# Kernel optimization log

Hardware: AMD Instinct MI355X
Metric: run time of the kernel (lower is better)

Reference implementation:

```python
import jax, jax.numpy as jnp
import numpy as np

B, S, D_IN, D_OUT = 4, 2048, 4096, 4096
R, E, SPLIT = 16, 4, 32
SCALING = 32.0 / 16.0  # lora_alpha / r


def setup_inputs() -> dict:
    key = jax.random.key(0)
    ks = jax.random.split(key, 9)
    x = jax.random.normal(ks[0], (B, S, D_IN), dtype=jnp.float32)
    w_base = jax.random.normal(ks[1], (D_OUT, D_IN), dtype=jnp.float32) * (1.0 / np.sqrt(D_IN))
    b_base = jax.random.normal(ks[2], (D_OUT,), dtype=jnp.float32) * 0.01
    w_router_img = jax.random.normal(ks[3], (E, D_IN), dtype=jnp.float32) * 1e-5
    b_router_img = jnp.zeros((E,), dtype=jnp.float32)
    w_router_text = jax.random.normal(ks[4], (E, D_IN), dtype=jnp.float32) * 1e-5
    b_router_text = jnp.zeros((E,), dtype=jnp.float32)
    # per-expert LoRA factors: A_e: [r, D_in], B_e: [D_out, r]
    lora_A = jax.random.normal(ks[5], (E, R, D_IN), dtype=jnp.float32) * (1.0 / np.sqrt(D_IN))
    lora_B = jax.random.normal(ks[6], (E, D_OUT, R), dtype=jnp.float32) * 0.02
    return {
        "x": x, "w_base": w_base, "b_base": b_base,
        "w_router_img": w_router_img, "b_router_img": b_router_img,
        "w_router_text": w_router_text, "b_router_text": b_router_text,
        "lora_A": lora_A, "lora_B": lora_B,
    }


def reference(x, w_base, b_base, w_router_img, b_router_img,
              w_router_text, b_router_text, lora_A, lora_B):
    # base linear: [B,S,D_out]
    base = jnp.einsum("bsd,od->bso", x, w_base) + b_base

    # modality routing: first SPLIT tokens are image, rest text
    x_img, x_text = x[:, :SPLIT], x[:, SPLIT:]
    logits_img = jnp.einsum("bsd,ed->bse", x_img, w_router_img) + b_router_img
    logits_text = jnp.einsum("bsd,ed->bse", x_text, w_router_text) + b_router_text
    gate = jax.nn.softmax(jnp.concatenate([logits_img, logits_text], axis=1), axis=-1)  # [B,S,E]

    # low-rank expert branches: h[b,s,e,r] = x @ A_e^T
    h = jnp.einsum("bsd,erd->bser", x, lora_A)
    h = h * gate[..., None]  # weight each expert's rank-r activation by its gate
    lora_out = jnp.einsum("bser,eor->bso", h, lora_B) * SCALING

    return base + lora_out
```

## Files before the change

kernel.cpp:

```cpp
#include <hip/hip_runtime.h>
#include <hip/hip_bf16.h>

#define D_IN   4096
#define D_OUT  4096
#define NTOK   8192
#define SEQ    2048
#define ER     64

typedef float        f32x4  __attribute__((ext_vector_type(4)));
typedef unsigned int u32x4  __attribute__((ext_vector_type(4)));
typedef unsigned int u32x2  __attribute__((ext_vector_type(2)));
typedef short        s16x8  __attribute__((ext_vector_type(8)));
typedef __bf16       bf16x8 __attribute__((ext_vector_type(8)));
typedef _Float16     f16x8  __attribute__((ext_vector_type(8)));

__device__ inline unsigned f2bf1(float f){
    unsigned u = __builtin_bit_cast(unsigned, f);
    return (u + 0x7fffu + ((u >> 16) & 1u)) >> 16;
}
__device__ inline unsigned pack2(float a, float b){ return f2bf1(a) | (f2bf1(b) << 16); }
__device__ inline f32x4 mfma_bf16(s16x8 a, s16x8 b, f32x4 c){
    return __builtin_amdgcn_mfma_f32_16x16x32_bf16(
        __builtin_bit_cast(bf16x8, a), __builtin_bit_cast(bf16x8, b), c, 0, 0, 0);
}
__device__ inline f32x4 mfma16(s16x8 a, s16x8 b, f32x4 c){
    return __builtin_amdgcn_mfma_f32_16x16x32_f16(
        __builtin_bit_cast(f16x8, a), __builtin_bit_cast(f16x8, b), c, 0, 0, 0);
}

__global__ __launch_bounds__(256) void convert_w_kernel(
    const float* __restrict__ w, _Float16* __restrict__ wh)
{
    size_t i = ((size_t)blockIdx.x * 256 + threadIdx.x) * 8;
    f32x4 a = *(const f32x4*)(w + i);
    f32x4 c = *(const f32x4*)(w + i + 4);
    f16x8 h;
    #pragma unroll
    for (int j = 0; j < 4; ++j){ h[j] = (_Float16)a[j]; h[4+j] = (_Float16)c[j]; }
    *(f16x8*)(wh + i) = h;
}

__global__ __launch_bounds__(256) void lora_c_kernel(
    const float* __restrict__ x,
    const float* __restrict__ wr_img, const float* __restrict__ br_img,
    const float* __restrict__ wr_txt, const float* __restrict__ br_txt,
    const float* __restrict__ lA,
    _Float16* __restrict__ xh, float* __restrict__ c_ws)
{
    __shared__ short xs[16][136];
    __shared__ short bs[80][136];
    __shared__ float lg[16][4];

    const int tid  = threadIdx.x;
    const int lane = tid & 63;
    const int wid  = tid >> 6;
    const int t0   = blockIdx.x * 16;
    const bool img = ((t0 % SEQ) < 32);
    const float* wrr = img ? wr_img : wr_txt;
    const float* br  = img ? br_img : br_txt;

    for (int idx = tid; idx < 816; idx += 256)
        ((unsigned*)&bs[68][0])[idx] = 0u;

    const int xr  = tid >> 4;
    const int xc8 = (tid & 15) * 8;
    const int lr  = tid >> 2;
    const int lc  = (tid & 3) * 4;
    const int rrow = tid >> 5;
    const int rcol = (tid & 31) * 4;

    f32x4 rx0, rx1, rb[8], rv = {0.f,0.f,0.f,0.f};
    rx0 = *(const f32x4*)(x + (size_t)(t0 + xr) * D_IN + xc8);
    rx1 = *(const f32x4*)(x + (size_t)(t0 + xr) * D_IN + xc8 + 4);
    #pragma unroll
    for (int j = 0; j < 8; ++j) rb[j] = *(const f32x4*)(lA + (size_t)lr * D_IN + lc + j*16);
    if (tid < 128) rv = *(const f32x4*)(wrr + (size_t)rrow * D_IN + rcol);

    f32x4 acc0 = {0,0,0,0}, accR0 = {0,0,0,0};
    const int fr = lane & 15, fq = lane >> 4;

    for (int ks = 0; ks < 32; ++ks){
        __syncthreads();
        *(u32x4*)&xs[xr][xc8] = (u32x4){pack2(rx0[0],rx0[1]), pack2(rx0[2],rx0[3]),
                                        pack2(rx1[0],rx1[1]), pack2(rx1[2],rx1[3])};
        #pragma unroll
        for (int j = 0; j < 8; ++j)
            *(u32x2*)&bs[lr][lc + j*16] = (u32x2){pack2(rb[j][0],rb[j][1]), pack2(rb[j][2],rb[j][3])};
        if (tid < 128)
            *(u32x2*)&bs[64 + rrow][rcol] = (u32x2){pack2(rv[0],rv[1]), pack2(rv[2],rv[3])};
        __syncthreads();
        {
            f16x8 h;
            #pragma unroll
            for (int j = 0; j < 4; ++j){ h[j] = (_Float16)rx0[j]; h[4+j] = (_Float16)rx1[j]; }
            *(f16x8*)(xh + (size_t)(t0 + xr) * D_IN + ks*128 + xc8) = h;
        }
        if (ks < 31){
            const int ko = (ks + 1) * 128;
            rx0 = *(const f32x4*)(x + (size_t)(t0 + xr) * D_IN + ko + xc8);
            rx1 = *(const f32x4*)(x + (size_t)(t0 + xr) * D_IN + ko + xc8 + 4);
            #pragma unroll
            for (int j = 0; j < 8; ++j) rb[j] = *(const f32x4*)(lA + (size_t)lr * D_IN + ko + lc + j*16);
            if (tid < 128) rv = *(const f32x4*)(wrr + (size_t)rrow * D_IN + ko + rcol);
        }
        #pragma unroll
        for (int kc = 0; kc < 4; ++kc){
            s16x8 a0 = *(const s16x8*)&xs[fr][kc*32 + fq*8];
            s16x8 b0 = *(const s16x8*)&bs[wid*16 + fr][kc*32 + fq*8];
            acc0 = mfma_bf16(a0, b0, acc0);
            if (wid == 0){
                s16x8 bR = *(const s16x8*)&bs[64 + fr][kc*32 + fq*8];
                accR0 = mfma_bf16(a0, bR, accR0);
            }
        }
    }

    __syncthreads();
    if (wid == 0 && fr < 4){
        #pragma unroll
        for (int r = 0; r < 4; ++r)
            lg[fq*4 + r][fr] = accR0[r] + br[fr];
    }
    __syncthreads();
    if (tid < 16){
        float l0 = lg[tid][0], l1 = lg[tid][1], l2 = lg[tid][2], l3 = lg[tid][3];
        float mx = fmaxf(fmaxf(l0, l1), fmaxf(l2, l3));
        float e0 = expf(l0 - mx), e1 = expf(l1 - mx), e2 = expf(l2 - mx), e3 = expf(l3 - mx);
        float inv = 2.0f / (e0 + e1 + e2 + e3);
        lg[tid][0] = e0 * inv; lg[tid][1] = e1 * inv;
        lg[tid][2] = e2 * inv; lg[tid][3] = e3 * inv;
    }
    __syncthreads();
    #pragma unroll
    for (int r = 0; r < 4; ++r){
        const int row0 = fq*4 + r;
        c_ws[(size_t)(t0 + row0) * ER + wid*16 + fr] = acc0[r] * lg[row0][wid];
    }
}

#define REG_A0 0
#define REG_A1 16384
#define REG_B0 32768
#define REG_B1 49152
#define BUFSZ  65536

__device__ inline void gload16(const void* g, void* l){
    __builtin_amdgcn_global_load_lds(
        (const __attribute__((address_space(1))) unsigned*)g,
        (__attribute__((address_space(3))) unsigned*)l, 16, 0, 0);
}
__device__ inline void stage_half_tile(const _Float16* gbase, char* lds, int tid){
    #pragma unroll
    for (int j = 0; j < 2; ++j){
        int q   = j*512 + tid;
        int row = q >> 3;
        int c7  = (q & 7) ^ (row & 7);
        gload16(gbase + (size_t)row * D_IN + c7*8, lds + q*16);
    }
}
__device__ inline s16x8 ldsfrag(const char* region, int row, int kc, int fq){
    int ch = ((kc << 2) + fq) ^ (row & 7);
    return *(const s16x8*)(region + row*128 + ch*16);
}
#define BAR()   __builtin_amdgcn_s_barrier()
#define LGKM0() asm volatile("s_waitcnt lgkmcnt(0)" ::: "memory")
#define PRIO(x) __builtin_amdgcn_s_setprio(x)

__global__ __launch_bounds__(512, 2) void main_gemm_kernel(
    const _Float16* __restrict__ xh, const _Float16* __restrict__ wh,
    const float* __restrict__ bias, const float* __restrict__ lB,
    const float* __restrict__ c_ws, float* __restrict__ out)
{
    __shared__ __align__(16) char smem[2 * BUFSZ];

    const int tid  = threadIdx.x;
    const int lane = tid & 63;
    const int wid  = tid >> 6;
    const int wr   = wid >> 2;
    const int wc   = wid & 3;
    const int fr   = lane & 15, fq = lane >> 4;

    const int bid = blockIdx.x;
    const int swz = (bid & 7) * 64 + (bid >> 3);
    const int mt  = swz & 31, nt = swz >> 5;
    const int m0  = mt * 256, n0 = nt * 256;

    const _Float16* gA0 = xh + (size_t)m0 * D_IN;
    const _Float16* gA1 = gA0 + (size_t)128 * D_IN;
    const _Float16* gB0 = wh + (size_t)n0 * D_IN;
    const _Float16* gB1 = gB0 + (size_t)128 * D_IN;

    stage_half_tile(gA0,      smem + REG_A0,         tid);
    stage_half_tile(gA1,      smem + REG_A1,         tid);
    stage_half_tile(gB0,      smem + REG_B0,         tid);
    stage_half_tile(gB1,      smem + REG_B1,         tid);
    stage_half_tile(gB0 + 64, smem + BUFSZ + REG_B0, tid);
    stage_half_tile(gA0 + 64, smem + BUFSZ + REG_A0, tid);
    stage_half_tile(gA1 + 64, smem + BUFSZ + REG_A1, tid);
    asm volatile("s_waitcnt vmcnt(6)" ::: "memory");
    BAR();

    f32x4 acc[8][4];
    #pragma unroll
    for (int mi = 0; mi < 8; ++mi)
        #pragma unroll
        for (int n = 0; n < 4; ++n) acc[mi][n] = (f32x4){0.f,0.f,0.f,0.f};

    const int bcol0 = (wc & 1) * 64;

    for (int it = 0; it < 32; ++it){
        const bool pred = (it < 31);
        #pragma unroll
        for (int hf = 0; hf < 2; ++hf){
            char* buf  = smem + hf * BUFSZ;
            char* obuf = smem + (hf ^ 1) * BUFSZ;
            const char* Ab = buf + wr * 16384;
            const char* Bb = buf + REG_B0 + (wc >> 1) * 16384;
            const size_t kP0 = (size_t)(2*it + 1 + hf) * 64;
            const size_t kN  = (size_t)(2*it + 2 + hf) * 64;
            const bool  prP0 = (hf == 0) ? true : pred;

            s16x8 af[4][2], blo[2][2], bhi[2][2];
            #pragma unroll
            for (int mi = 0; mi < 4; ++mi)
                #pragma unroll
                for (int kc = 0; kc < 2; ++kc)
                    af[mi][kc] = ldsfrag(Ab, mi*16 + fr, kc, fq);
            #pragma unroll
            for (int nn = 0; nn < 2; ++nn)
                #pragma unroll
                for (int kc = 0; kc < 2; ++kc)
                    blo[nn][kc] = ldsfrag(Bb, bcol0 + nn*16 + fr, kc, fq);
            if (prP0) stage_half_tile(gB1 + kP0, obuf + REG_B1, tid);
            BAR(); LGKM0(); PRIO(1);
            #pragma unroll
            for (int mi = 0; mi < 4; ++mi)
                #pragma unroll
                for (int nn = 0; nn < 2; ++nn)
                    #pragma unroll
                    for (int kc = 0; kc < 2; ++kc)
                        acc[mi][nn] = mfma16(af[mi][kc], blo[nn][kc], acc[mi][nn]);
            PRIO(0); BAR();
            #pragma unroll
            for (int nn = 0; nn < 2; ++nn)
                #pragma unroll
                for (int kc = 0; kc < 2; ++kc)
                    bhi[nn][kc] = ldsfrag(Bb, bcol0 + 32 + nn*16 + fr, kc, fq);
            BAR(); LGKM0(); PRIO(1);
            #pragma unroll
            for (int mi = 0; mi < 4; ++mi)
                #pragma unroll
                for (int nn = 0; nn < 2; ++nn)
                    #pragma unroll
                    for (int kc = 0; kc < 2; ++kc)
                        acc[mi][2+nn] = mfma16(af[mi][kc], bhi[nn][kc], acc[mi][2+nn]);
            PRIO(0); BAR();
            #pragma unroll
            for (int mi = 0; mi < 4; ++mi)
                #pragma unroll
                for (int kc = 0; kc < 2; ++kc)
                    af[mi][kc] = ldsfrag(Ab, 64 + mi*16 + fr, kc, fq);
            if (pred) stage_half_tile(gB0 + kN, buf + REG_B0, tid);
            BAR(); LGKM0(); PRIO(1);
            #pragma unroll
            for (int mi = 0; mi < 4; ++mi)
                #pragma unroll
                for (int nn = 0; nn < 2; ++nn)
                    #pragma unroll
                    for (int kc = 0; kc < 2; ++kc)
                        acc[4+mi][2+nn] = mfma16(af[mi][kc], bhi[nn][kc], acc[4+mi][2+nn]);
            PRIO(0); BAR();
            if (pred){
                stage_half_tile(gA0 + kN, buf + REG_A0, tid);
                stage_half_tile(gA1 + kN, buf + REG_A1, tid);
            }
            BAR(); PRIO(1);
            #pragma unroll
            for (int mi = 0; mi < 4; ++mi)
                #pragma unroll
                for (int nn = 0; nn < 2; ++nn)
                    #pragma unroll
                    for (int kc = 0; kc < 2; ++kc)
                        acc[4+mi][nn] = mfma16(af[mi][kc], blo[nn][kc], acc[4+mi][nn]);
            PRIO(0);
            if (pred)           asm volatile("s_waitcnt vmcnt(6)" ::: "memory");
            else if (hf == 0)   asm volatile("s_waitcnt vmcnt(0)" ::: "memory");
            BAR();
        }
    }

    #pragma unroll
    for (int k2 = 0; k2 < 4; ++k2){
        int q = tid + k2*512;
        int row = q >> 3, cc = q & 7;
        const float* cs = c_ws + (size_t)(m0 + row) * ER + cc*8;
        f32x4 v0 = *(const f32x4*)cs;
        f32x4 v1 = *(const f32x4*)(cs + 4);
        f16x8 h;
        #pragma unroll
        for (int j = 0; j < 4; ++j){ h[j] = (_Float16)v0[j]; h[4+j] = (_Float16)v1[j]; }
        *(s16x8*)(smem + row*128 + (cc ^ (row & 7))*16) = __builtin_bit_cast(s16x8, h);
    }
    #pragma unroll
    for (int k2 = 0; k2 < 4; ++k2){
        int q = tid + k2*512;
        int row = q >> 3, cc = q & 7;
        int e = cc >> 1, r0 = (cc & 1) * 8;
        const float* bsrc = lB + (size_t)e * D_OUT * 16 + (size_t)(n0 + row) * 16 + r0;
        f32x4 v0 = *(const f32x4*)bsrc;
        f32x4 v1 = *(const f32x4*)(bsrc + 4);
        f16x8 h;
        #pragma unroll
        for (int j = 0; j < 4; ++j){ h[j] = (_Float16)v0[j]; h[4+j] = (_Float16)v1[j]; }
        *(s16x8*)(smem + 32768 + row*128 + (cc ^ (row & 7))*16) = __builtin_bit_cast(s16x8, h);
    }
    __syncthreads();

    #pragma unroll
    for (int kc = 0; kc < 2; ++kc){
        s16x8 btf[4];
        #pragma unroll
        for (int n = 0; n < 4; ++n)
            btf[n] = ldsfrag(smem + 32768, wc*64 + n*16 + fr, kc, fq);
        #pragma unroll
        for (int mi = 0; mi < 8; ++mi){
            s16x8 cf = ldsfrag(smem, wr*128 + mi*16 + fr, kc, fq);
            #pragma unroll
            for (int n = 0; n < 4; ++n)
                acc[mi][n] = mfma16(cf, btf[n], acc[mi][n]);
        }
    }

    #pragma unroll
    for (int n = 0; n < 4; ++n){
        const int col = n0 + wc*64 + n*16 + fr;
        const float bb = bias[col];
        #pragma unroll
        for (int mi = 0; mi < 8; ++mi){
            const int row = m0 + wr*128 + mi*16 + fq*4;
            #pragma unroll
            for (int r = 0; r < 4; ++r)
                out[(size_t)(row + r) * D_OUT + col] = acc[mi][n][r] + bb;
        }
    }
}

extern "C" void kernel_launch(void* const* d_in, const int* in_sizes, int n_in,
                              void* d_out, int out_size, void* d_ws, size_t ws_size,
                              hipStream_t stream)
{
    const float* x      = (const float*)d_in[0];
    const float* w_base = (const float*)d_in[1];
    const float* b_base = (const float*)d_in[2];
    const float* wr_img = (const float*)d_in[3];
    const float* br_img = (const float*)d_in[4];
    const float* wr_txt = (const float*)d_in[5];
    const float* br_txt = (const float*)d_in[6];
    const float* lA     = (const float*)d_in[7];
    const float* lB     = (const float*)d_in[8];
    float* out = (float*)d_out;

    char* ws = (char*)d_ws;
    float*    c_ws = (float*)ws;
    _Float16* xh   = (_Float16*)(ws + (size_t)(2<<20));
    _Float16* wh   = (_Float16*)(ws + (size_t)(66<<20));

    convert_w_kernel<<<dim3(8192), dim3(256), 0, stream>>>(w_base, wh);
    lora_c_kernel<<<dim3(NTOK/16), dim3(256), 0, stream>>>(
        x, wr_img, br_img, wr_txt, br_txt, lA, xh, c_ws);
    main_gemm_kernel<<<dim3(512), dim3(512), 0, stream>>>(
        xh, wh, b_base, lB, c_ws, out);
}
```

Before: 566.3 us.

## Split LoRA projection over K slices and switch main GEMM to 32x32 MFMA

The LoRA/router projection is split into 16 K-slices with 64-token tiles, writing fp16 partials and fp32 router partials. A new gate kernel reduces them, applies the softmax gate and emits an fp16 coefficient matrix. The main GEMM moves from 16x16x32 to 32x32x16 f16 MFMA with a remapped fragment layout and epilogue, and loads the fp16 coefficients directly. This aims to raise parallelism in the small LoRA stage and cut LDS fragment traffic per MFMA, at the cost of an extra kernel launch, partial-sum workspace traffic and fp16 rounding of the partials.

New measurement: 581.3 us. 2.7% more time.

```diff
diff --git a/kernel.cpp b/kernel.cpp
--- a/kernel.cpp
+++ b/kernel.cpp
@@ -6,13 +6,16 @@
 #define NTOK   8192
 #define SEQ    2048
 #define ER     64
+#define NSLICE 16
 
 typedef float        f32x4  __attribute__((ext_vector_type(4)));
+typedef float        f32x16 __attribute__((ext_vector_type(16)));
 typedef unsigned int u32x4  __attribute__((ext_vector_type(4)));
 typedef unsigned int u32x2  __attribute__((ext_vector_type(2)));
 typedef short        s16x8  __attribute__((ext_vector_type(8)));
 typedef __bf16       bf16x8 __attribute__((ext_vector_type(8)));
 typedef _Float16     f16x8  __attribute__((ext_vector_type(8)));
+typedef _Float16     f16x4  __attribute__((ext_vector_type(4)));
 
 __device__ inline unsigned f2bf1(float f){
     unsigned u = __builtin_bit_cast(unsigned, f);
@@ -23,8 +26,8 @@
     return __builtin_amdgcn_mfma_f32_16x16x32_bf16(
         __builtin_bit_cast(bf16x8, a), __builtin_bit_cast(bf16x8, b), c, 0, 0, 0);
 }
-__device__ inline f32x4 mfma16(s16x8 a, s16x8 b, f32x4 c){
-    return __builtin_amdgcn_mfma_f32_16x16x32_f16(
+__device__ inline f32x16 mfma32(s16x8 a, s16x8 b, f32x16 c){
+    return __builtin_amdgcn_mfma_f32_32x32x16_f16(
         __builtin_bit_cast(f16x8, a), __builtin_bit_cast(f16x8, b), c, 0, 0, 0);
 }
 
@@ -40,102 +43,123 @@
     *(f16x8*)(wh + i) = h;
 }
 
-__global__ __launch_bounds__(256) void lora_c_kernel(
+__global__ __launch_bounds__(256) void lora_part_kernel(
     const float* __restrict__ x,
-    const float* __restrict__ wr_img, const float* __restrict__ br_img,
-    const float* __restrict__ wr_txt, const float* __restrict__ br_txt,
+    const float* __restrict__ wr_img, const float* __restrict__ wr_txt,
     const float* __restrict__ lA,
-    _Float16* __restrict__ xh, float* __restrict__ c_ws)
-{
-    __shared__ short xs[16][136];
-    __shared__ short bs[80][136];
-    __shared__ float lg[16][4];
+    _Float16* __restrict__ xh, _Float16* __restrict__ pc, float* __restrict__ plg)
+{
+    __shared__ short xs[64][264];
 
     const int tid  = threadIdx.x;
     const int lane = tid & 63;
     const int wid  = tid >> 6;
-    const int t0   = blockIdx.x * 16;
-    const bool img = ((t0 % SEQ) < 32);
-    const float* wrr = img ? wr_img : wr_txt;
-    const float* br  = img ? br_img : br_txt;
-
-    for (int idx = tid; idx < 816; idx += 256)
-        ((unsigned*)&bs[68][0])[idx] = 0u;
-
-    const int xr  = tid >> 4;
-    const int xc8 = (tid & 15) * 8;
-    const int lr  = tid >> 2;
-    const int lc  = (tid & 3) * 4;
-    const int rrow = tid >> 5;
-    const int rcol = (tid & 31) * 4;
-
-    f32x4 rx0, rx1, rb[8], rv = {0.f,0.f,0.f,0.f};
-    rx0 = *(const f32x4*)(x + (size_t)(t0 + xr) * D_IN + xc8);
-    rx1 = *(const f32x4*)(x + (size_t)(t0 + xr) * D_IN + xc8 + 4);
-    #pragma unroll
-    for (int j = 0; j < 8; ++j) rb[j] = *(const f32x4*)(lA + (size_t)lr * D_IN + lc + j*16);
-    if (tid < 128) rv = *(const f32x4*)(wrr + (size_t)rrow * D_IN + rcol);
-
-    f32x4 acc0 = {0,0,0,0}, accR0 = {0,0,0,0};
+    const int mt   = blockIdx.x & 127;
+    const int sl   = blockIdx.x >> 7;
+    const int t0   = mt * 64;
+    const int kb   = sl * 256;
+
+    #pragma unroll
+    for (int j = 0; j < 8; ++j){
+        int q   = tid + j * 256;
+        int row = q >> 5, cc = q & 31;
+        const float* src = x + (size_t)(t0 + row) * D_IN + kb + cc * 8;
+        f32x4 v0 = *(const f32x4*)src;
+        f32x4 v1 = *(const f32x4*)(src + 4);
+        f16x8 h;
+        #pragma unroll
+        for (int jj = 0; jj < 4; ++jj){ h[jj] = (_Float16)v0[jj]; h[4+jj] = (_Float16)v1[jj]; }
+        *(f16x8*)(xh + (size_t)(t0 + row) * D_IN + kb + cc * 8) = h;
+        *(u32x4*)&xs[row][cc * 8] = (u32x4){pack2(v0[0],v0[1]), pack2(v0[2],v0[3]),
+                                            pack2(v1[0],v1[1]), pack2(v1[2],v1[3])};
+    }
+    __syncthreads();
+
     const int fr = lane & 15, fq = lane >> 4;
-
-    for (int ks = 0; ks < 32; ++ks){
-        __syncthreads();
-        *(u32x4*)&xs[xr][xc8] = (u32x4){pack2(rx0[0],rx0[1]), pack2(rx0[2],rx0[3]),
-                                        pack2(rx1[0],rx1[1]), pack2(rx1[2],rx1[3])};
-        #pragma unroll
-        for (int j = 0; j < 8; ++j)
-            *(u32x2*)&bs[lr][lc + j*16] = (u32x2){pack2(rb[j][0],rb[j][1]), pack2(rb[j][2],rb[j][3])};
-        if (tid < 128)
-            *(u32x2*)&bs[64 + rrow][rcol] = (u32x2){pack2(rv[0],rv[1]), pack2(rv[2],rv[3])};
-        __syncthreads();
-        {
-            f16x8 h;
-            #pragma unroll
-            for (int j = 0; j < 4; ++j){ h[j] = (_Float16)rx0[j]; h[4+j] = (_Float16)rx1[j]; }
-            *(f16x8*)(xh + (size_t)(t0 + xr) * D_IN + ks*128 + xc8) = h;
+    f32x4 acc[4]  = {{0,0,0,0},{0,0,0,0},{0,0,0,0},{0,0,0,0}};
+    f32x4 accR[4] = {{0,0,0,0},{0,0,0,0},{0,0,0,0},{0,0,0,0}};
+
+    const float* bp = lA + (size_t)(wid * 16 + fr) * D_IN + kb + fq * 8;
+    const float* rp = (fr < 4) ? wr_img + (size_t)fr * D_IN + kb + fq * 8
+                               : wr_txt + (size_t)(fr - 4) * D_IN + kb + fq * 8;
+
+    #pragma unroll
+    for (int ks = 0; ks < 8; ++ks){
+        f32x4 b0 = *(const f32x4*)(bp + ks * 32);
+        f32x4 b1 = *(const f32x4*)(bp + ks * 32 + 4);
+        s16x8 bw = __builtin_bit_cast(s16x8,
+            (u32x4){pack2(b0[0],b0[1]), pack2(b0[2],b0[3]),
+                    pack2(b1[0],b1[1]), pack2(b1[2],b1[3])});
+        s16x8 bR = __builtin_bit_cast(s16x8, (u32x4){0u,0u,0u,0u});
+        if (wid == 0 && fr < 8){
+            f32x4 r0 = *(const f32x4*)(rp + ks * 32);
+            f32x4 r1 = *(const f32x4*)(rp + ks * 32 + 4);
+            bR = __builtin_bit_cast(s16x8,
+                (u32x4){pack2(r0[0],r0[1]), pack2(r0[2],r0[3]),
+                        pack2(r1[0],r1[1]), pack2(r1[2],r1[3])});
         }
-        if (ks < 31){
-            const int ko = (ks + 1) * 128;
-            rx0 = *(const f32x4*)(x + (size_t)(t0 + xr) * D_IN + ko + xc8);
-            rx1 = *(const f32x4*)(x + (size_t)(t0 + xr) * D_IN + ko + xc8 + 4);
-            #pragma unroll
-            for (int j = 0; j < 8; ++j) rb[j] = *(const f32x4*)(lA + (size_t)lr * D_IN + ko + lc + j*16);
-            if (tid < 128) rv = *(const f32x4*)(wrr + (size_t)rrow * D_IN + ko + rcol);
+        #pragma unroll
+        for (int mi = 0; mi < 4; ++mi){
+            s16x8 a = *(const s16x8*)&xs[mi * 16 + fr][ks * 32 + fq * 8];
+            acc[mi] = mfma_bf16(a, bw, acc[mi]);
+            if (wid == 0) accR[mi] = mfma_bf16(a, bR, accR[mi]);
         }
-        #pragma unroll
-        for (int kc = 0; kc < 4; ++kc){
-            s16x8 a0 = *(const s16x8*)&xs[fr][kc*32 + fq*8];
-            s16x8 b0 = *(const s16x8*)&bs[wid*16 + fr][kc*32 + fq*8];
-            acc0 = mfma_bf16(a0, b0, acc0);
-            if (wid == 0){
-                s16x8 bR = *(const s16x8*)&bs[64 + fr][kc*32 + fq*8];
-                accR0 = mfma_bf16(a0, bR, accR0);
-            }
-        }
-    }
-
-    __syncthreads();
-    if (wid == 0 && fr < 4){
+    }
+
+    _Float16* pcb = pc + ((size_t)sl * NTOK + t0) * ER;
+    #pragma unroll
+    for (int mi = 0; mi < 4; ++mi)
         #pragma unroll
         for (int r = 0; r < 4; ++r)
-            lg[fq*4 + r][fr] = accR0[r] + br[fr];
-    }
-    __syncthreads();
-    if (tid < 16){
-        float l0 = lg[tid][0], l1 = lg[tid][1], l2 = lg[tid][2], l3 = lg[tid][3];
-        float mx = fmaxf(fmaxf(l0, l1), fmaxf(l2, l3));
-        float e0 = expf(l0 - mx), e1 = expf(l1 - mx), e2 = expf(l2 - mx), e3 = expf(l3 - mx);
-        float inv = 2.0f / (e0 + e1 + e2 + e3);
-        lg[tid][0] = e0 * inv; lg[tid][1] = e1 * inv;
-        lg[tid][2] = e2 * inv; lg[tid][3] = e3 * inv;
-    }
-    __syncthreads();
-    #pragma unroll
-    for (int r = 0; r < 4; ++r){
-        const int row0 = fq*4 + r;
-        c_ws[(size_t)(t0 + row0) * ER + wid*16 + fr] = acc0[r] * lg[row0][wid];
-    }
+            pcb[(size_t)(mi * 16 + fq * 4 + r) * ER + wid * 16 + fr] = (_Float16)acc[mi][r];
+
+    if (wid == 0 && fr < 8){
+        float* pb = plg + ((size_t)sl * NTOK + t0) * 8;
+        #pragma unroll
+        for (int mi = 0; mi < 4; ++mi)
+            #pragma unroll
+            for (int r = 0; r < 4; ++r)
+                pb[(size_t)(mi * 16 + fq * 4 + r) * 8 + fr] = accR[mi][r];
+    }
+}
+
+__global__ __launch_bounds__(256) void lora_gate_kernel(
+    const _Float16* __restrict__ pc, const float* __restrict__ plg,
+    const float* __restrict__ br_img, const float* __restrict__ br_txt,
+    _Float16* __restrict__ c_h)
+{
+    const int tid = threadIdx.x;
+    const int row = blockIdx.x * 16 + (tid >> 4);
+    const int erq = (tid & 15) * 4;
+
+    float s0=0.f, s1=0.f, s2=0.f, s3=0.f;
+    float lg0=0,lg1=0,lg2=0,lg3=0,lg4=0,lg5=0,lg6=0,lg7=0;
+    #pragma unroll
+    for (int sl = 0; sl < NSLICE; ++sl){
+        f16x4 v = *(const f16x4*)(pc + ((size_t)sl * NTOK + row) * ER + erq);
+        s0 += (float)v[0]; s1 += (float)v[1]; s2 += (float)v[2]; s3 += (float)v[3];
+        const float* q = plg + ((size_t)sl * NTOK + row) * 8;
+        f32x4 a = *(const f32x4*)q;
+        f32x4 b = *(const f32x4*)(q + 4);
+        lg0 += a[0]; lg1 += a[1]; lg2 += a[2]; lg3 += a[3];
+        lg4 += b[0]; lg5 += b[1]; lg6 += b[2]; lg7 += b[3];
+    }
+    const bool img = (row & (SEQ - 1)) < 32;
+    const float* br = img ? br_img : br_txt;
+    float l0 = (img ? lg0 : lg4) + br[0];
+    float l1 = (img ? lg1 : lg5) + br[1];
+    float l2 = (img ? lg2 : lg6) + br[2];
+    float l3 = (img ? lg3 : lg7) + br[3];
+    float mx = fmaxf(fmaxf(l0, l1), fmaxf(l2, l3));
+    float e0 = expf(l0 - mx), e1 = expf(l1 - mx), e2 = expf(l2 - mx), e3 = expf(l3 - mx);
+    float inv = 2.0f / (e0 + e1 + e2 + e3);
+    const int e = erq >> 4;
+    float g = (e == 0 ? e0 : e == 1 ? e1 : e == 2 ? e2 : e3) * inv;
+
+    f16x4 o;
+    o[0] = (_Float16)(s0 * g); o[1] = (_Float16)(s1 * g);
+    o[2] = (_Float16)(s2 * g); o[3] = (_Float16)(s3 * g);
+    *(f16x4*)(c_h + (size_t)row * ER + erq) = o;
 }
 
 #define REG_A0 0
@@ -158,8 +182,8 @@
         gload16(gbase + (size_t)row * D_IN + c7*8, lds + q*16);
     }
 }
-__device__ inline s16x8 ldsfrag(const char* region, int row, int kc, int fq){
-    int ch = ((kc << 2) + fq) ^ (row & 7);
+__device__ inline s16x8 ldsfrag32(const char* region, int row, int ks, int kh){
+    int ch = ((ks << 1) | kh) ^ (row & 7);
     return *(const s16x8*)(region + row*128 + ch*16);
 }
 #define BAR()   __builtin_amdgcn_s_barrier()
@@ -169,7 +193,7 @@
 __global__ __launch_bounds__(512, 2) void main_gemm_kernel(
     const _Float16* __restrict__ xh, const _Float16* __restrict__ wh,
     const float* __restrict__ bias, const float* __restrict__ lB,
-    const float* __restrict__ c_ws, float* __restrict__ out)
+    const _Float16* __restrict__ c_h, float* __restrict__ out)
 {
     __shared__ __align__(16) char smem[2 * BUFSZ];
 
@@ -178,7 +202,8 @@
     const int wid  = tid >> 6;
     const int wr   = wid >> 2;
     const int wc   = wid & 3;
-    const int fr   = lane & 15, fq = lane >> 4;
+    const int l31  = lane & 31;
+    const int kh   = lane >> 5;
 
     const int bid = blockIdx.x;
     const int swz = (bid & 7) * 64 + (bid >> 3);
@@ -200,11 +225,13 @@
     asm volatile("s_waitcnt vmcnt(6)" ::: "memory");
     BAR();
 
-    f32x4 acc[8][4];
-    #pragma unroll
-    for (int mi = 0; mi < 8; ++mi)
-        #pragma unroll
-        for (int n = 0; n < 4; ++n) acc[mi][n] = (f32x4){0.f,0.f,0.f,0.f};
+    f32x16 acc[4][2];
+    #pragma unroll
+    for (int tr = 0; tr < 4; ++tr)
+        #pragma unroll
+        for (int tc = 0; tc < 2; ++tc)
+            #pragma unroll
+            for (int v = 0; v < 16; ++v) acc[tr][tc][v] = 0.f;
 
     const int bcol0 = (wc & 1) * 64;
 
@@ -220,55 +247,45 @@
             const size_t kN  = (size_t)(2*it + 2 + hf) * 64;
             const bool  prP0 = (hf == 0) ? true : pred;
 
-            s16x8 af[4][2], blo[2][2], bhi[2][2];
-            #pragma unroll
-            for (int mi = 0; mi < 4; ++mi)
-                #pragma unroll
-                for (int kc = 0; kc < 2; ++kc)
-                    af[mi][kc] = ldsfrag(Ab, mi*16 + fr, kc, fq);
-            #pragma unroll
-            for (int nn = 0; nn < 2; ++nn)
-                #pragma unroll
-                for (int kc = 0; kc < 2; ++kc)
-                    blo[nn][kc] = ldsfrag(Bb, bcol0 + nn*16 + fr, kc, fq);
+            s16x8 af[2][4], blo[4], bhi[4];
+            #pragma unroll
+            for (int tr = 0; tr < 2; ++tr)
+                #pragma unroll
+                for (int ks = 0; ks < 4; ++ks)
+                    af[tr][ks] = ldsfrag32(Ab, tr*32 + l31, ks, kh);
+            #pragma unroll
+            for (int ks = 0; ks < 4; ++ks)
+                blo[ks] = ldsfrag32(Bb, bcol0 + l31, ks, kh);
             if (prP0) stage_half_tile(gB1 + kP0, obuf + REG_B1, tid);
             BAR(); LGKM0(); PRIO(1);
             #pragma unroll
-            for (int mi = 0; mi < 4; ++mi)
-                #pragma unroll
-                for (int nn = 0; nn < 2; ++nn)
-                    #pragma unroll
-                    for (int kc = 0; kc < 2; ++kc)
-                        acc[mi][nn] = mfma16(af[mi][kc], blo[nn][kc], acc[mi][nn]);
+            for (int tr = 0; tr < 2; ++tr)
+                #pragma unroll
+                for (int ks = 0; ks < 4; ++ks)
+                    acc[tr][0] = mfma32(af[tr][ks], blo[ks], acc[tr][0]);
             PRIO(0); BAR();
             #pragma unroll
-            for (int nn = 0; nn < 2; ++nn)
-                #pragma unroll
-                for (int kc = 0; kc < 2; ++kc)
-                    bhi[nn][kc] = ldsfrag(Bb, bcol0 + 32 + nn*16 + fr, kc, fq);
+            for (int ks = 0; ks < 4; ++ks)
+                bhi[ks] = ldsfrag32(Bb, bcol0 + 32 + l31, ks, kh);
             BAR(); LGKM0(); PRIO(1);
             #pragma unroll
-            for (int mi = 0; mi < 4; ++mi)
-                #pragma unroll
-                for (int nn = 0; nn < 2; ++nn)
-                    #pragma unroll
-                    for (int kc = 0; kc < 2; ++kc)
-                        acc[mi][2+nn] = mfma16(af[mi][kc], bhi[nn][kc], acc[mi][2+nn]);
+            for (int tr = 0; tr < 2; ++tr)
+                #pragma unroll
+                for (int ks = 0; ks < 4; ++ks)
+                    acc[tr][1] = mfma32(af[tr][ks], bhi[ks], acc[tr][1]);
             PRIO(0); BAR();
             #pragma unroll
-            for (int mi = 0; mi < 4; ++mi)
-                #pragma unroll
-                for (int kc = 0; kc < 2; ++kc)
-                    af[mi][kc] = ldsfrag(Ab, 64 + mi*16 + fr, kc, fq);
+            for (int tr = 0; tr < 2; ++tr)
+                #pragma unroll
+                for (int ks = 0; ks < 4; ++ks)
+                    af[tr][ks] = ldsfrag32(Ab, 64 + tr*32 + l31, ks, kh);
             if (pred) stage_half_tile(gB0 + kN, buf + REG_B0, tid);
             BAR(); LGKM0(); PRIO(1);
             #pragma unroll
-            for (int mi = 0; mi < 4; ++mi)
-                #pragma unroll
-                for (int nn = 0; nn < 2; ++nn)
-                    #pragma unroll
-                    for (int kc = 0; kc < 2; ++kc)
-                        acc[4+mi][2+nn] = mfma16(af[mi][kc], bhi[nn][kc], acc[4+mi][2+nn]);
+            for (int tr = 0; tr < 2; ++tr)
+                #pragma unroll
+                for (int ks = 0; ks < 4; ++ks)
+                    acc[2+tr][1] = mfma32(af[tr][ks], bhi[ks], acc[2+tr][1]);
             PRIO(0); BAR();
             if (pred){
                 stage_half_tile(gA0 + kN, buf + REG_A0, tid);
@@ -276,12 +293,10 @@
             }
             BAR(); PRIO(1);
             #pragma unroll
-            for (int mi = 0; mi < 4; ++mi)
-                #pragma unroll
-                for (int nn = 0; nn < 2; ++nn)
-                    #pragma unroll
-                    for (int kc = 0; kc < 2; ++kc)
-                        acc[4+mi][nn] = mfma16(af[mi][kc], blo[nn][kc], acc[4+mi][nn]);
+            for (int tr = 0; tr < 2; ++tr)
+                #pragma unroll
+                for (int ks = 0; ks < 4; ++ks)
+                    acc[2+tr][0] = mfma32(af[tr][ks], blo[ks], acc[2+tr][0]);
             PRIO(0);
             if (pred)           asm volatile("s_waitcnt vmcnt(6)" ::: "memory");
             else if (hf == 0)   asm volatile("s_waitcnt vmcnt(0)" ::: "memory");
@@ -293,13 +308,8 @@
     for (int k2 = 0; k2 < 4; ++k2){
         int q = tid + k2*512;
         int row = q >> 3, cc = q & 7;
-        const float* cs = c_ws + (size_t)(m0 + row) * ER + cc*8;
-        f32x4 v0 = *(const f32x4*)cs;
-        f32x4 v1 = *(const f32x4*)(cs + 4);
-        f16x8 h;
-        #pragma unroll
-        for (int j = 0; j < 4; ++j){ h[j] = (_Float16)v0[j]; h[4+j] = (_Float16)v1[j]; }
-        *(s16x8*)(smem + row*128 + (cc ^ (row & 7))*16) = __builtin_bit_cast(s16x8, h);
+        s16x8 v = *(const s16x8*)(c_h + (size_t)(m0 + row) * ER + cc*8);
+        *(s16x8*)(smem + row*128 + ((cc ^ (row & 7)))*16) = v;
     }
     #pragma unroll
     for (int k2 = 0; k2 < 4; ++k2){
@@ -312,36 +322,44 @@
         f16x8 h;
         #pragma unroll
         for (int j = 0; j < 4; ++j){ h[j] = (_Float16)v0[j]; h[4+j] = (_Float16)v1[j]; }
-        *(s16x8*)(smem + 32768 + row*128 + (cc ^ (row & 7))*16) = __builtin_bit_cast(s16x8, h);
+        *(s16x8*)(smem + 32768 + row*128 + ((cc ^ (row & 7)))*16) = __builtin_bit_cast(s16x8, h);
     }
     __syncthreads();
 
-    #pragma unroll
-    for (int kc = 0; kc < 2; ++kc){
-        s16x8 btf[4];
-        #pragma unroll
-        for (int n = 0; n < 4; ++n)
-            btf[n] = ldsfrag(smem + 32768, wc*64 + n*16 + fr, kc, fq);
-        #pragma unroll
-        for (int mi = 0; mi < 8; ++mi){
-            s16x8 cf = ldsfrag(smem, wr*128 + mi*16 + fr, kc, fq);
-            #pragma unroll
-            for (int n = 0; n < 4; ++n)
-                acc[mi][n] = mfma16(cf, btf[n], acc[mi][n]);
+    {
+        s16x8 btf[2][4];
+        #pragma unroll
+        for (int tc = 0; tc < 2; ++tc)
+            #pragma unroll
+            for (int ks = 0; ks < 4; ++ks)
+                btf[tc][ks] = ldsfrag32(smem + 32768, wc*64 + tc*32 + l31, ks, kh);
+        #pragma unroll
+        for (int tr = 0; tr < 4; ++tr){
+            s16x8 cf[4];
+            #pragma unroll
+            for (int ks = 0; ks < 4; ++ks)
+                cf[ks] = ldsfrag32(smem, wr*128 + tr*32 + l31, ks, kh);
+            #pragma unroll
+            for (int tc = 0; tc < 2; ++tc)
+                #pragma unroll
+                for (int ks = 0; ks < 4; ++ks)
+                    acc[tr][tc] = mfma32(cf[ks], btf[tc][ks], acc[tr][tc]);
         }
     }
 
-    #pragma unroll
-    for (int n = 0; n < 4; ++n){
-        const int col = n0 + wc*64 + n*16 + fr;
-        const float bb = bias[col];
-        #pragma unroll
-        for (int mi = 0; mi < 8; ++mi){
-            const int row = m0 + wr*128 + mi*16 + fq*4;
-            #pragma unroll
-            for (int r = 0; r < 4; ++r)
-                out[(size_t)(row + r) * D_OUT + col] = acc[mi][n][r] + bb;
-        }
+    const int colb = n0 + wc*64 + l31;
+    const int rowb = m0 + wr*128 + kh*4;
+    #pragma unroll
+    for (int tc = 0; tc < 2; ++tc){
+        const float bb = bias[colb + tc*32];
+        #pragma unroll
+        for (int tr = 0; tr < 4; ++tr)
+            #pragma unroll
+            for (int g = 0; g < 4; ++g)
+                #pragma unroll
+                for (int r = 0; r < 4; ++r)
+                    out[(size_t)(rowb + tr*32 + g*8 + r) * D_OUT + colb + tc*32]
+                        = acc[tr][tc][g*4 + r] + bb;
     }
 }
 
@@ -361,13 +379,17 @@
     float* out = (float*)d_out;
 
     char* ws = (char*)d_ws;
-    float*    c_ws = (float*)ws;
-    _Float16* xh   = (_Float16*)(ws + (size_t)(2<<20));
-    _Float16* wh   = (_Float16*)(ws + (size_t)(66<<20));
-
+    _Float16* c_h = (_Float16*)ws;
+    _Float16* xh  = (_Float16*)(ws + (size_t)( 2 << 20));
+    _Float16* wh  = (_Float16*)(ws + (size_t)(66 << 20));
+    _Float16* pc  = (_Float16*)(ws + (size_t)(98 << 20));
+    float*    plg = (float*)   (ws + (size_t)(114 << 20));
+
+    lora_part_kernel<<<dim3(128 * NSLICE), dim3(256), 0, stream>>>(
+        x, wr_img, wr_txt, lA, xh, pc, plg);
     convert_w_kernel<<<dim3(8192), dim3(256), 0, stream>>>(w_base, wh);
-    lora_c_kernel<<<dim3(NTOK/16), dim3(256), 0, stream>>>(
-        x, wr_img, br_img, wr_txt, br_txt, lA, xh, c_ws);
+    lora_gate_kernel<<<dim3(NTOK / 16), dim3(256), 0, stream>>>(
+        pc, plg, br_img, br_txt, c_h);
     main_gemm_kernel<<<dim3(512), dim3(512), 0, stream>>>(
-        xh, wh, b_base, lB, c_ws, out);
-}
+        xh, wh, b_base, lB, c_h, out);
+}
```
